# Kernel tuning notes

Hardware: AMD Instinct MI355X
Metric: run time of the kernel (lower is better)

## Reference

```python
import jax, jax.numpy as jnp
import numpy as np

EPS_NORM = 1e-12
EPS_COS = 1e-8

def _l2norm(x, axis):
    n = jnp.linalg.norm(x, axis=axis, keepdims=True)
    return x / jnp.maximum(n, EPS_NORM)

def setup_inputs() -> dict:
    key = jax.random.key(0)
    k1, k2, k3 = jax.random.split(key, 3)
    B, C, H, W, M = 16, 512, 32, 32, 1024
    query = jax.random.normal(k1, (B, C, H, W), dtype=jnp.float32)
    keys = jax.random.normal(k2, (M, C), dtype=jnp.float32)
    entropy = jax.random.uniform(k3, (B * H * W, 1), dtype=jnp.float32) + 1e-3
    return {"query": query, "keys": keys, "entropy": entropy}

def reference(query, keys, entropy):
    B, C, H, W = query.shape
    M = keys.shape[0]
    N = B * H * W
    # F.normalize over channel dim, then BCHW -> BHWC -> [N, C]
    q = _l2norm(query, axis=1)
    q = jnp.transpose(q, (0, 2, 3, 1))
    qr = q.reshape(N, C)

    # get_score: softmax over queries (axis 0) and over memory (axis 1)
    score = jnp.einsum('nd,md->nm', qr, keys)  # [N, M]
    sq = jax.nn.softmax(score, axis=0)
    sm = jax.nn.softmax(score, axis=1)

    # ---- memory_loss ----
    argm = jnp.argmax(sm, axis=1)               # topk(k=1) over memory
    closest = keys[argm]                         # [N, C]
    eye = jnp.eye(M, dtype=keys.dtype)
    gram = keys @ keys.T
    diversity_loss = jnp.sum((gram * (1.0 - eye)) ** 2) / (M * M - M)
    cos = jnp.sum(qr * closest, axis=1) / jnp.maximum(
        jnp.linalg.norm(qr, axis=1) * jnp.linalg.norm(closest, axis=1), EPS_COS)
    similarity_loss = jnp.dot(1.0 - cos, entropy[:, 0])  # CosineEmbeddingLoss(target=1) . entropy

    # ---- read ----
    concat_memory = jax.lax.stop_gradient(sm) @ keys    # [N, C]
    updated_query = jnp.concatenate([qr, concat_memory], axis=1)  # [N, 2C]
    updated_query = updated_query.reshape(B, H, W, 2 * C)
    updated_query = jnp.transpose(updated_query, (0, 3, 1, 2))    # [B, 2C, H, W]

    # ---- update (train=True) ----
    g = argm                                     # gathering indices (argmax == topk1)
    sq_d = jax.lax.stop_gradient(sq)
    ent_d = jax.lax.stop_gradient(entropy[:, 0])
    colmax = jnp.max(sq_d, axis=0)               # max score per memory slot [M]
    w = (sq_d[jnp.arange(N), g] / colmax[g]) * (ent_d / jnp.max(ent_d))  # [N]
    query_update = jax.ops.segment_sum(w[:, None] * qr, g, num_segments=M)  # [M, C]
    updated_memory = _l2norm(query_update + jax.lax.stop_gradient(keys), axis=1)
    gram2 = updated_memory @ updated_memory.T
    diversity_loss_updated = jnp.sum((gram2 * (1.0 - eye)) ** 2) / (M * M - M)
    updated_memory = jax.lax.stop_gradient(updated_memory)

    return (updated_query, updated_memory, sq, sm, diversity_loss_updated, similarity_loss)
```

## Files before the change

kernel.cpp:

```cpp
#include <hip/hip_runtime.h>

typedef unsigned int  u32;
typedef unsigned short u16;
typedef __bf16 bf16x8 __attribute__((ext_vector_type(8)));
typedef float  f32x4  __attribute__((ext_vector_type(4)));

#define O1 16777216
#define O2 17301504
#define O3 34078720
#define O4 50855936
#define O5 50855937

#define WS_QHI   0u
#define WS_QLO   16777216u
#define WS_KHI   33554432u
#define WS_KLO   34603008u
#define WS_KT    35651584u
#define WS_KNORM 36700160u
#define WS_CNT   36704256u
#define WS_OFFS  36708352u
#define WS_CUR   36712704u
#define WS_RN    36769792u
#define WS_PMAX  36835328u
#define WS_PSUM  36900864u
#define WS_CMAX  36966400u
#define WS_CSUM  36970496u
#define WS_ARGM  36974592u
#define WS_WGT   37040128u
#define WS_SCAL  39202816u

__device__ __forceinline__ u16 bf_rne(float f){
  u32 u = __float_as_uint(f);
  u32 r = u + 0x7fffu + ((u >> 16) & 1u);
  return (u16)(r >> 16);
}
__device__ __forceinline__ float bf_f(u16 h){ return __uint_as_float(((u32)h) << 16); }

__device__ __forceinline__ void glds16(const void* g, void* l){
  __builtin_amdgcn_global_load_lds((const __attribute__((address_space(1))) u32*)g,
                                   (__attribute__((address_space(3))) u32*)l, 16, 0, 0);
}

__global__ void k_init(u32* count, float* scal){
  int i = blockIdx.x*256 + threadIdx.x;
  if (i < 1024) count[i] = 0u;
  if (i < 16) scal[i] = 0.f;
}

__global__ __launch_bounds__(64) void k_keys(const float* __restrict__ keys,
    u16* __restrict__ khi, u16* __restrict__ klo, float* __restrict__ knorm){
  int m = blockIdx.x, l = threadIdx.x;
  const float* kr = keys + (size_t)m*512 + l*8;
  float f[8];
  #pragma unroll
  for (int i=0;i<8;i++) f[i] = kr[i];
  float ss = 0.f;
  #pragma unroll
  for (int i=0;i<8;i++) ss += f[i]*f[i];
  for (int o=32;o>0;o>>=1) ss += __shfl_xor(ss,o);
  if (l == 0) knorm[m] = sqrtf(ss);
  u32 hh[4], ll[4];
  #pragma unroll
  for (int i=0;i<4;i++){
    u16 h0 = bf_rne(f[2*i]);   u16 l0 = bf_rne(f[2*i]   - bf_f(h0));
    u16 h1 = bf_rne(f[2*i+1]); u16 l1 = bf_rne(f[2*i+1] - bf_f(h1));
    hh[i] = (u32)h0 | ((u32)h1<<16);
    ll[i] = (u32)l0 | ((u32)l1<<16);
  }
  *(uint4*)&khi[(size_t)m*512 + l*8] = make_uint4(hh[0],hh[1],hh[2],hh[3]);
  *(uint4*)&klo[(size_t)m*512 + l*8] = make_uint4(ll[0],ll[1],ll[2],ll[3]);
}

__global__ __launch_bounds__(256) void k_keysT(const float* __restrict__ keys, u16* __restrict__ kT){
  __shared__ float t2[64*65];
  int m0 = blockIdx.x*64, c0 = blockIdx.y*64;
  int t = threadIdx.x; int j = t & 63; int ig = t >> 6;
  #pragma unroll 4
  for (int ii=0; ii<16; ++ii){
    int i = ig*16 + ii;
    t2[i*65 + j] = keys[(size_t)(m0+i)*512 + c0 + j];
  }
  __syncthreads();
  #pragma unroll 4
  for (int ii=0; ii<16; ++ii){
    int i = ig*16 + ii;
    kT[(size_t)(c0+i)*1024 + m0 + j] = bf_rne(t2[j*65 + i]);
  }
}

__global__ __launch_bounds__(256) void k_maxent(const float* __restrict__ ent, float* scal){
  int i = blockIdx.x*512 + threadIdx.x;
  float v = fmaxf(ent[i], ent[i + 256]);
  for (int o=32;o>0;o>>=1) v = fmaxf(v, __shfl_xor(v,o));
  __shared__ float r4[4];
  if ((threadIdx.x & 63) == 0) r4[threadIdx.x>>6] = v;
  __syncthreads();
  if (threadIdx.x == 0){
    float mx = fmaxf(fmaxf(r4[0],r4[1]), fmaxf(r4[2],r4[3]));
    atomicMax((u32*)(scal + 1), __float_as_uint(mx));
  }
}

__global__ __launch_bounds__(256) void k_phaseA(const float* __restrict__ query, float* __restrict__ out0,
    u16* __restrict__ qhi, u16* __restrict__ qlo, float* __restrict__ rn_g){
  __shared__ float tile[64*65];
  __shared__ float red[256];
  __shared__ float sinv[64];
  int bx = blockIdx.x; int b = bx >> 4; int hw0 = (bx & 15)*64;
  int t = threadIdx.x; int hw = t & 63; int cg = t >> 6;
  const float* qb = query + (size_t)b*524288 + hw0 + hw;
  float p = 0.f;
  for (int c = cg; c < 512; c += 4){ float v = qb[(size_t)c*1024]; p += v*v; }
  red[cg*64 + hw] = p;
  __syncthreads();
  if (t < 64){
    float ss = red[t] + red[64+t] + red[128+t] + red[192+t];
    float nrm = sqrtf(ss);
    float inv = 1.0f / fmaxf(nrm, 1e-12f);
    sinv[t] = inv;
    rn_g[b*1024 + hw0 + t] = nrm * inv;
  }
  __syncthreads();
  int nl = t >> 2, cq = t & 3;
  int n = b*1024 + hw0 + nl;
  float invv = sinv[hw];
  for (int cb = 0; cb < 8; ++cb){
    int cbase = cb*64;
    #pragma unroll 4
    for (int i = 0; i < 16; ++i){
      int cl = cg*16 + i;
      int c = cbase + cl;
      float v = query[(size_t)b*524288 + (size_t)c*1024 + hw0 + hw] * invv;
      tile[cl*65 + hw] = v;
      out0[(size_t)b*1048576 + (size_t)c*1024 + hw0 + hw] = v;
    }
    __syncthreads();
    u32 hh[8], ll[8];
    #pragma unroll
    for (int p2 = 0; p2 < 8; ++p2){
      float f0 = tile[(cq*16 + p2*2)*65 + nl];
      float f1 = tile[(cq*16 + p2*2 + 1)*65 + nl];
      u16 h0 = bf_rne(f0); u16 lo0 = bf_rne(f0 - bf_f(h0));
      u16 h1 = bf_rne(f1); u16 lo1 = bf_rne(f1 - bf_f(h1));
      hh[p2] = (u32)h0 | ((u32)h1 << 16);
      ll[p2] = (u32)lo0 | ((u32)lo1 << 16);
    }
    size_t base = (size_t)n*512 + cbase + cq*16;
    *(uint4*)&qhi[base]     = make_uint4(hh[0],hh[1],hh[2],hh[3]);
    *(uint4*)&qhi[base + 8] = make_uint4(hh[4],hh[5],hh[6],hh[7]);
    *(uint4*)&qlo[base]     = make_uint4(ll[0],ll[1],ll[2],ll[3]);
    *(uint4*)&qlo[base + 8] = make_uint4(ll[4],ll[5],ll[6],ll[7]);
    __syncthreads();
  }
}

__global__ __launch_bounds__(256) void k_score(const u16* __restrict__ qhi, const u16* __restrict__ qlo,
    const u16* __restrict__ khi, const u16* __restrict__ klo, float* __restrict__ S){
  __shared__ u16 sAh[8192], sAl[8192], sBh[8192], sBl[8192];
  int tid = threadIdx.x;
  int nt = blockIdx.x >> 3, mt = blockIdx.x & 7;
  int nBase = nt*128, mBase = mt*128;
  int wave = tid >> 6, lane = tid & 63;
  int rw = (wave>>1)*64, cw = (wave&1)*64;
  int m16 = lane & 15, q4 = lane >> 4;
  f32x4 acc[4][4] = {};
  int srow = tid >> 3, sg = tid & 7;
  for (int kit = 0; kit < 8; ++kit){
    int k0 = kit*64;
    #pragma unroll
    for (int it = 0; it < 4; ++it){
      int row = it*32 + srow;
      int gsw = (sg ^ (row & 7)) * 8;
      int lo = it*2048 + tid*8;
      glds16(qhi + (size_t)(nBase + row)*512 + k0 + gsw, &sAh[lo]);
      glds16(qlo + (size_t)(nBase + row)*512 + k0 + gsw, &sAl[lo]);
      glds16(khi + (size_t)(mBase + row)*512 + k0 + gsw, &sBh[lo]);
      glds16(klo + (size_t)(mBase + row)*512 + k0 + gsw, &sBl[lo]);
    }
    __syncthreads();
    #pragma unroll
    for (int ks = 0; ks < 2; ++ks){
      bf16x8 a0[4], a1[4], b0[4], b1[4];
      int g = ks*4 + q4;
      #pragma unroll
      for (int i=0;i<4;i++){
        int r = rw + i*16 + m16;
        int off = r*64 + (g ^ (r&7))*8;
        a0[i] = *(const bf16x8*)&sAh[off];
        a1[i] = *(const bf16x8*)&sAl[off];
      }
      #pragma unroll
      for (int j=0;j<4;j++){
        int r = cw + j*16 + m16;
        int off = r*64 + (g ^ (r&7))*8;
        b0[j] = *(const bf16x8*)&sBh[off];
        b1[j] = *(const bf16x8*)&sBl[off];
      }
      #pragma unroll
      for (int i=0;i<4;i++)
        #pragma unroll
        for (int j=0;j<4;j++){
          acc[i][j] = __builtin_amdgcn_mfma_f32_16x16x32_bf16(a0[i], b0[j], acc[i][j], 0,0,0);
          acc[i][j] = __builtin_amdgcn_mfma_f32_16x16x32_bf16(a0[i], b1[j], acc[i][j], 0,0,0);
          acc[i][j] = __builtin_amdgcn_mfma_f32_16x16x32_bf16(a1[i], b0[j], acc[i][j], 0,0,0);
        }
    }
    __syncthreads();
  }
  #pragma unroll
  for (int i=0;i<4;i++){
    int rbase = nBase + rw + i*16 + q4*4;
    #pragma unroll
    for (int j=0;j<4;j++){
      int col = mBase + cw + j*16 + m16;
      #pragma unroll
      for (int r=0;r<4;r++)
        S[(size_t)(rbase + r)*1024 + col] = acc[i][j][r];
    }
  }
}

__global__ __launch_bounds__(256) void k_colstat(const float* __restrict__ S,
    float* __restrict__ pmax, float* __restrict__ psum){
  int c = threadIdx.x & 63;
  int col = blockIdx.x*64 + c;
  int rg = threadIdx.x >> 6;
  int row0 = blockIdx.y*1024 + rg*256;
  float m = -3.4e38f, s = 0.f;
  for (int r=0;r<256;r++){
    float v = S[(size_t)(row0+r)*1024 + col];
    if (v > m){ s = s*__expf(m - v) + 1.f; m = v; }
    else s += __expf(v - m);
  }
  __shared__ float lm[256], ls[256];
  lm[rg*64 + c] = m; ls[rg*64 + c] = s;
  __syncthreads();
  if (threadIdx.x < 64){
    int t = threadIdx.x;
    float M = lm[t];
    for (int g2=1; g2<4; ++g2) M = fmaxf(M, lm[g2*64+t]);
    float st = 0.f;
    for (int g2=0; g2<4; ++g2) st += ls[g2*64+t]*__expf(lm[g2*64+t] - M);
    pmax[blockIdx.y*1024 + blockIdx.x*64 + t] = M;
    psum[blockIdx.y*1024 + blockIdx.x*64 + t] = st;
  }
}

__global__ void k_colfin(const float* __restrict__ pmax, const float* __restrict__ psum,
    float* __restrict__ cmax, float* __restrict__ csum){
  int col = blockIdx.x*256 + threadIdx.x;
  float M = -3.4e38f, s = 0.f;
  for (int ch=0; ch<16; ++ch){
    float mi = pmax[ch*1024 + col], si = psum[ch*1024 + col];
    float nm = fmaxf(M, mi);
    s = s*__expf(M - nm) + si*__expf(mi - nm);
    M = nm;
  }
  cmax[col] = M; csum[col] = s;
}

__global__ __launch_bounds__(256) void k_row(float* __restrict__ S, float* __restrict__ sm,
    const float* __restrict__ cmax, const float* __restrict__ csum,
    const float* __restrict__ rn, const float* __restrict__ knorm,
    const float* __restrict__ ent, const float* __restrict__ scal,
    int* __restrict__ argm, float* __restrict__ wgt, u32* __restrict__ count,
    float* __restrict__ sim_acc){
  int wave = threadIdx.x >> 6, lane = threadIdx.x & 63;
  int n = blockIdx.x*4 + wave;
  float4 v[4];
  const float4* Sr = (const float4*)(S + (size_t)n*1024);
  #pragma unroll
  for (int j=0;j<4;j++) v[j] = Sr[j*64 + lane];
  float m = -3.4e38f; int gi = 0;
  #pragma unroll
  for (int j=0;j<4;j++){
    int c0 = j*256 + lane*4;
    if (v[j].x > m){ m=v[j].x; gi=c0; }
    if (v[j].y > m){ m=v[j].y; gi=c0+1; }
    if (v[j].z > m){ m=v[j].z; gi=c0+2; }
    if (v[j].w > m){ m=v[j].w; gi=c0+3; }
  }
  for (int o=32;o>0;o>>=1){
    float om = __shfl_xor(m,o); int oi = __shfl_xor(gi,o);
    if (om > m || (om == m && oi < gi)){ m = om; gi = oi; }
  }
  float4 e[4]; float s = 0.f;
  #pragma unroll
  for (int j=0;j<4;j++){
    e[j].x = __expf(v[j].x - m); e[j].y = __expf(v[j].y - m);
    e[j].z = __expf(v[j].z - m); e[j].w = __expf(v[j].w - m);
    s += e[j].x + e[j].y + e[j].z + e[j].w;
  }
  for (int o=32;o>0;o>>=1) s += __shfl_xor(s,o);
  float ri = 1.f/s;
  float4* smr = (float4*)(sm + (size_t)n*1024);
  #pragma unroll
  for (int j=0;j<4;j++){
    float4 t2; t2.x=e[j].x*ri; t2.y=e[j].y*ri; t2.z=e[j].z*ri; t2.w=e[j].w*ri;
    smr[j*64 + lane] = t2;
  }
  float4* sqr = (float4*)(S + (size_t)n*1024);
  #pragma unroll
  for (int j=0;j<4;j++){
    int c0 = j*256 + lane*4;
    float4 cm = *(const float4*)(cmax + c0);
    float4 cs = *(const float4*)(csum + c0);
    float4 q;
    q.x = __expf(v[j].x - cm.x)/cs.x;
    q.y = __expf(v[j].y - cm.y)/cs.y;
    q.z = __expf(v[j].z - cm.z)/cs.z;
    q.w = __expf(v[j].w - cm.w)/cs.w;
    sqr[j*64 + lane] = q;
  }
  __shared__ float simw[4];
  if (lane == 0){
    float en = ent[n];
    float cosv = m / fmaxf(rn[n]*knorm[gi], 1e-8f);
    simw[wave] = (1.f - cosv)*en;
    float w = __expf(m - cmax[gi]) * en / scal[1];
    wgt[n] = w; argm[n] = gi;
    atomicAdd(&count[gi], 1u);
  }
  __syncthreads();
  if (threadIdx.x == 0)
    atomicAdd(sim_acc, simw[0]+simw[1]+simw[2]+simw[3]);
}

__global__ __launch_bounds__(256) void k_scan(const u32* __restrict__ count,
    u32* __restrict__ offs, u32* __restrict__ cursor){
  int t = threadIdx.x;
  u32 v0 = count[t*4], v1 = count[t*4+1], v2 = count[t*4+2], v3 = count[t*4+3];
  u32 s = v0+v1+v2+v3;
  u32 x = s;
  for (int o=1;o<64;o<<=1){ u32 y = __shfl_up(x,o); if ((t&63) >= o) x += y; }
  __shared__ u32 wsum[4];
  if ((t&63) == 63) wsum[t>>6] = x;
  __syncthreads();
  u32 wb = 0;
  for (int wv=0; wv < (t>>6); ++wv) wb += wsum[wv];
  u32 excl = wb + x - s;
  u32 o0 = excl, o1 = excl+v0, o2 = excl+v0+v1, o3 = excl+v0+v1+v2;
  offs[t*4]=o0; offs[t*4+1]=o1; offs[t*4+2]=o2; offs[t*4+3]=o3;
  cursor[t*4]=o0; cursor[t*4+1]=o1; cursor[t*4+2]=o2; cursor[t*4+3]=o3;
  if (t == 255) offs[1024] = 16384u;
}

__global__ __launch_bounds__(256) void k_bucket(const int* __restrict__ argm,
    u32* __restrict__ cursor, u32* __restrict__ list){
  int n = blockIdx.x*256 + threadIdx.x;
  int g = argm[n];
  u32 pos = atomicAdd(&cursor[g], 1u);
  list[pos] = n;
}

__global__ __launch_bounds__(128) void k_gather(const u16* __restrict__ qhi, const u16* __restrict__ qlo,
    const u32* __restrict__ offs, const u32* __restrict__ list, const float* __restrict__ wgt,
    const float* __restrict__ keys, float* __restrict__ out1, float* __restrict__ scal){
  int m = blockIdx.x, t = threadIdx.x;
  int c0 = t*4;
  float a0=0.f,a1=0.f,a2=0.f,a3=0.f;
  u32 beg = offs[m], end = offs[m+1];
  for (u32 r = beg; r < end; ++r){
    int n = (int)list[r];
    float w = wgt[n];
    uint2 hh = *(const uint2*)&qhi[(size_t)n*512 + c0];
    uint2 ll = *(const uint2*)&qlo[(size_t)n*512 + c0];
    float f0 = bf_f((u16)(hh.x & 0xffffu)) + bf_f((u16)(ll.x & 0xffffu));
    float f1 = bf_f((u16)(hh.x >> 16))     + bf_f((u16)(ll.x >> 16));
    float f2 = bf_f((u16)(hh.y & 0xffffu)) + bf_f((u16)(ll.y & 0xffffu));
    float f3 = bf_f((u16)(hh.y >> 16))     + bf_f((u16)(ll.y >> 16));
    a0 += w*f0; a1 += w*f1; a2 += w*f2; a3 += w*f3;
  }
  float4 k4 = *(const float4*)(keys + (size_t)m*512 + c0);
  float u0 = a0 + k4.x, u1 = a1 + k4.y, u2 = a2 + k4.z, u3 = a3 + k4.w;
  float ss = u0*u0 + u1*u1 + u2*u2 + u3*u3;
  for (int o=32;o>0;o>>=1) ss += __shfl_xor(ss,o);
  __shared__ float r2[2];
  if ((t&63) == 0) r2[t>>6] = ss;
  __syncthreads();
  float tot = r2[0] + r2[1];
  float inv = 1.f / fmaxf(sqrtf(tot), 1e-12f);
  float4 o4; o4.x=u0*inv; o4.y=u1*inv; o4.z=u2*inv; o4.w=u3*inv;
  *(float4*)(out1 + (size_t)m*512 + c0) = o4;
  if (t == 0){
    float s2 = tot*inv*inv;
    atomicAdd(scal + 3, s2*s2);
  }
}

__global__ __launch_bounds__(256) void k_concat(const u16* __restrict__ kT, const float* __restrict__ sm,
    float* __restrict__ out0){
  __shared__ u16 sA[8192];
  __shared__ u16 sB[128*72];
  int tid = threadIdx.x;
  int ct = blockIdx.x & 3, nt = blockIdx.x >> 2;
  int cBase = ct*128, nBase = nt*128;
  int wave = tid>>6, lane = tid&63;
  int rw = (wave>>1)*64, cw = (wave&1)*64;
  int m16 = lane&15, q4 = lane>>4;
  f32x4 acc[4][4] = {};
  int srow = tid>>3, sg = tid&7;
  int nl = tid>>1, half = tid&1;
  for (int kit=0; kit<16; ++kit){
    int k0 = kit*64;
    #pragma unroll
    for (int it=0; it<4; ++it){
      int row = it*32 + srow;
      int gsw = (sg ^ (row & 7)) * 8;
      glds16(kT + (size_t)(cBase + row)*1024 + k0 + gsw, &sA[it*2048 + tid*8]);
    }
    {
      const float* src = sm + (size_t)(nBase + nl)*1024 + k0 + half*32;
      float4 f[8];
      #pragma unroll
      for (int q=0;q<8;q++) f[q] = *(const float4*)(src + q*4);
      u16* dst = &sB[nl*72 + half*32];
      #pragma unroll
      for (int q=0;q<4;q++){
        const float* fp = (const float*)&f[q*2];
        u32 w0 = (u32)bf_rne(fp[0]) | ((u32)bf_rne(fp[1])<<16);
        u32 w1 = (u32)bf_rne(fp[2]) | ((u32)bf_rne(fp[3])<<16);
        u32 w2 = (u32)bf_rne(fp[4]) | ((u32)bf_rne(fp[5])<<16);
        u32 w3 = (u32)bf_rne(fp[6]) | ((u32)bf_rne(fp[7])<<16);
        *(uint4*)(dst + q*8) = make_uint4(w0,w1,w2,w3);
      }
    }
    __syncthreads();
    #pragma unroll
    for (int ks=0; ks<2; ++ks){
      bf16x8 a[4], b[4];
      int g = ks*4 + q4;
      #pragma unroll
      for (int i=0;i<4;i++){
        int r = rw + i*16 + m16;
        a[i] = *(const bf16x8*)&sA[r*64 + (g ^ (r&7))*8];
      }
      #pragma unroll
      for (int j=0;j<4;j++){
        int r = cw + j*16 + m16;
        b[j] = *(const bf16x8*)&sB[r*72 + ks*32 + q4*8];
      }
      #pragma unroll
      for (int i=0;i<4;i++)
        #pragma unroll
        for (int j=0;j<4;j++)
          acc[i][j] = __builtin_amdgcn_mfma_f32_16x16x32_bf16(a[i], b[j], acc[i][j], 0,0,0);
    }
    __syncthreads();
  }
  #pragma unroll
  for (int i=0;i<4;i++){
    int c = cBase + rw + i*16 + q4*4;
    #pragma unroll
    for (int j=0;j<4;j++){
      int n = nBase + cw + j*16 + m16;
      int b2 = n >> 10, hw = n & 1023;
      #pragma unroll
      for (int r=0;r<4;r++)
        out0[(size_t)b2*1048576 + (size_t)(512 + c + r)*1024 + hw] = acc[i][j][r];
    }
  }
}

__global__ __launch_bounds__(256) void k_gram(const float* __restrict__ U, float* __restrict__ scal){
  __shared__ float Ua[64*34], Ub[64*34];
  int bx = blockIdx.x & 15, by = blockIdx.x >> 4;
  int t = threadIdx.x;
  int c1 = (t >> 4)*2, c2 = (t & 15)*2;
  float d00=0,d01=0,d10=0,d11=0;
  for (int ch=0; ch<16; ++ch){
    #pragma unroll
    for (int j=0;j<8;j++){
      int flat = j*256 + t;
      int ml = flat >> 5, c = flat & 31;
      Ua[ml*34 + c] = U[(size_t)(ch*64 + ml)*512 + bx*32 + c];
      Ub[ml*34 + c] = U[(size_t)(ch*64 + ml)*512 + by*32 + c];
    }
    __syncthreads();
    #pragma unroll 8
    for (int ml=0; ml<64; ++ml){
      float2 a = *(const float2*)&Ua[ml*34 + c1];
      float2 b = *(const float2*)&Ub[ml*34 + c2];
      d00 += a.x*b.x; d01 += a.x*b.y; d10 += a.y*b.x; d11 += a.y*b.y;
    }
    __syncthreads();
  }
  float loc = d00*d00 + d01*d01 + d10*d10 + d11*d11;
  for (int o=32;o>0;o>>=1) loc += __shfl_xor(loc,o);
  __shared__ float r4[4];
  if ((t&63) == 0) r4[t>>6] = loc;
  __syncthreads();
  if (t == 0) atomicAdd(scal + 2, r4[0]+r4[1]+r4[2]+r4[3]);
}

__global__ void k_final(const float* __restrict__ scal, float* __restrict__ out){
  out[O4] = (scal[2] - scal[3]) * (1.0f/1047552.0f);
  out[O5] = scal[0];
}

extern "C" void kernel_launch(void* const* d_in, const int* in_sizes, int n_in,
                              void* d_out, int out_size, void* d_ws, size_t ws_size,
                              hipStream_t stream) {
  const float* query = (const float*)d_in[0];
  const float* keys  = (const float*)d_in[1];
  const float* ent   = (const float*)d_in[2];
  float* out  = (float*)d_out;
  char*  ws   = (char*)d_ws;

  u16*   qhi   = (u16*)(ws + WS_QHI);
  u16*   qlo   = (u16*)(ws + WS_QLO);
  u16*   khi   = (u16*)(ws + WS_KHI);
  u16*   klo   = (u16*)(ws + WS_KLO);
  u16*   kT    = (u16*)(ws + WS_KT);
  float* knorm = (float*)(ws + WS_KNORM);
  u32*   count = (u32*)(ws + WS_CNT);
  u32*   offs  = (u32*)(ws + WS_OFFS);
  u32*   cursor= (u32*)(ws + WS_CUR);
  float* rn    = (float*)(ws + WS_RN);
  float* pmax  = (float*)(ws + WS_PMAX);
  float* psum  = (float*)(ws + WS_PSUM);
  float* cmax  = (float*)(ws + WS_CMAX);
  float* csum  = (float*)(ws + WS_CSUM);
  int*   argm  = (int*)(ws + WS_ARGM);
  float* wgt   = (float*)(ws + WS_WGT);
  float* scal  = (float*)(ws + WS_SCAL);
  u32*   list  = (u32*)(ws + WS_PMAX);

  float* S   = out + O2;
  float* sm  = out + O3;
  float* um  = out + O1;

  k_init   <<<4,    256, 0, stream>>>(count, scal);
  k_keys   <<<1024,  64, 0, stream>>>(keys, khi, klo, knorm);
  k_keysT  <<<dim3(16,8), 256, 0, stream>>>(keys, kT);
  k_maxent <<<32,   256, 0, stream>>>(ent, scal);
  k_phaseA <<<256,  256, 0, stream>>>(query, out, qhi, qlo, rn);
  k_score  <<<1024, 256, 0, stream>>>(qhi, qlo, khi, klo, S);
  k_colstat<<<dim3(16,16), 256, 0, stream>>>(S, pmax, psum);
  k_colfin <<<4,    256, 0, stream>>>(pmax, psum, cmax, csum);
  k_row    <<<4096, 256, 0, stream>>>(S, sm, cmax, csum, rn, knorm, ent, scal, argm, wgt, count, scal );
  k_scan   <<<1,    256, 0, stream>>>(count, offs, cursor);
  k_bucket <<<64,   256, 0, stream>>>(argm, cursor, list);
  k_gather <<<1024, 128, 0, stream>>>(qhi, qlo, offs, list, wgt, keys, um, scal);
  k_concat <<<512,  256, 0, stream>>>(kT, sm, out);
  k_gram   <<<256,  256, 0, stream>>>(um, scal);
  k_final  <<<1,      1, 0, stream>>>(scal, out);
}
```

Baseline: 588.9 us.

## Fuse column softmax stats into score GEMM epilogue; feed concat with bf16 sm copy

Per-tile column max and sum-of-exp are now computed in the k_score epilogue from the accumulators and written as 128 partial chunks. This removes the separate k_colstat pass that re-read the full 64MB score matrix. k_row also writes a bf16 copy of sm, so k_concat can load it directly into LDS with async global_load_lds instead of reading fp32 and converting inside the GEMM loop. The cost is an extra 32MB bf16 write, a longer k_colfin reduction over 128 chunks, and a heavier epilogue in k_score.

```diff
diff --git a/kernel.cpp b/kernel.cpp
--- a/kernel.cpp
+++ b/kernel.cpp
@@ -22,12 +22,14 @@
 #define WS_CUR   36712704u
 #define WS_RN    36769792u
 #define WS_PMAX  36835328u
-#define WS_PSUM  36900864u
 #define WS_CMAX  36966400u
 #define WS_CSUM  36970496u
 #define WS_ARGM  36974592u
 #define WS_WGT   37040128u
 #define WS_SCAL  39202816u
+#define WS_PM2   39203840u
+#define WS_PS2   39728128u
+#define WS_SM16  40252416u
 
 __device__ __forceinline__ u16 bf_rne(float f){
   u32 u = __float_as_uint(f);
@@ -155,7 +157,8 @@
 }
 
 __global__ __launch_bounds__(256) void k_score(const u16* __restrict__ qhi, const u16* __restrict__ qlo,
-    const u16* __restrict__ khi, const u16* __restrict__ klo, float* __restrict__ S){
+    const u16* __restrict__ khi, const u16* __restrict__ klo, float* __restrict__ S,
+    float* __restrict__ pm2, float* __restrict__ ps2){
   __shared__ u16 sAh[8192], sAl[8192], sBh[8192], sBl[8192];
   int tid = threadIdx.x;
   int nt = blockIdx.x >> 3, mt = blockIdx.x & 7;
@@ -218,40 +221,50 @@
         S[(size_t)(rbase + r)*1024 + col] = acc[i][j][r];
     }
   }
-}
-
-__global__ __launch_bounds__(256) void k_colstat(const float* __restrict__ S,
-    float* __restrict__ pmax, float* __restrict__ psum){
-  int c = threadIdx.x & 63;
-  int col = blockIdx.x*64 + c;
-  int rg = threadIdx.x >> 6;
-  int row0 = blockIdx.y*1024 + rg*256;
-  float m = -3.4e38f, s = 0.f;
-  for (int r=0;r<256;r++){
-    float v = S[(size_t)(row0+r)*1024 + col];
-    if (v > m){ s = s*__expf(m - v) + 1.f; m = v; }
-    else s += __expf(v - m);
-  }
-  __shared__ float lm[256], ls[256];
-  lm[rg*64 + c] = m; ls[rg*64 + c] = s;
-  __syncthreads();
-  if (threadIdx.x < 64){
-    int t = threadIdx.x;
-    float M = lm[t];
-    for (int g2=1; g2<4; ++g2) M = fmaxf(M, lm[g2*64+t]);
-    float st = 0.f;
-    for (int g2=0; g2<4; ++g2) st += ls[g2*64+t]*__expf(lm[g2*64+t] - M);
-    pmax[blockIdx.y*1024 + blockIdx.x*64 + t] = M;
-    psum[blockIdx.y*1024 + blockIdx.x*64 + t] = st;
-  }
-}
-
-__global__ void k_colfin(const float* __restrict__ pmax, const float* __restrict__ psum,
+  float* lm = (float*)sAh;
+  float* ls = lm + 256;
+  #pragma unroll
+  for (int j=0;j<4;j++){
+    float cm = -3.4e38f;
+    #pragma unroll
+    for (int i=0;i<4;i++)
+      #pragma unroll
+      for (int r=0;r<4;r++) cm = fmaxf(cm, acc[i][j][r]);
+    cm = fmaxf(cm, __shfl_xor(cm, 16));
+    cm = fmaxf(cm, __shfl_xor(cm, 32));
+    float cs = 0.f;
+    #pragma unroll
+    for (int i=0;i<4;i++)
+      #pragma unroll
+      for (int r=0;r<4;r++) cs += __expf(acc[i][j][r] - cm);
+    cs += __shfl_xor(cs, 16);
+    cs += __shfl_xor(cs, 32);
+    if (lane < 16){
+      lm[(wave*4 + j)*16 + m16] = cm;
+      ls[(wave*4 + j)*16 + m16] = cs;
+    }
+  }
+  __syncthreads();
+  if (tid < 128){
+    int w = tid >> 6;
+    int x = tid & 63;
+    int j = x >> 4, c16 = x & 15;
+    float m0 = lm[(w*4 + j)*16 + c16],     s0 = ls[(w*4 + j)*16 + c16];
+    float m1 = lm[((w+2)*4 + j)*16 + c16], s1 = ls[((w+2)*4 + j)*16 + c16];
+    float M  = fmaxf(m0, m1);
+    float Sv = s0*__expf(m0 - M) + s1*__expf(m1 - M);
+    int col = mBase + w*64 + j*16 + c16;
+    pm2[nt*1024 + col] = M;
+    ps2[nt*1024 + col] = Sv;
+  }
+}
+
+__global__ void k_colfin(const float* __restrict__ pm2, const float* __restrict__ ps2,
     float* __restrict__ cmax, float* __restrict__ csum){
   int col = blockIdx.x*256 + threadIdx.x;
   float M = -3.4e38f, s = 0.f;
-  for (int ch=0; ch<16; ++ch){
-    float mi = pmax[ch*1024 + col], si = psum[ch*1024 + col];
+  for (int ch=0; ch<128; ++ch){
+    float mi = pm2[ch*1024 + col], si = ps2[ch*1024 + col];
     float nm = fmaxf(M, mi);
     s = s*__expf(M - nm) + si*__expf(mi - nm);
     M = nm;
@@ -260,6 +273,7 @@
 }
 
 __global__ __launch_bounds__(256) void k_row(float* __restrict__ S, float* __restrict__ sm,
+    u16* __restrict__ sm16,
     const float* __restrict__ cmax, const float* __restrict__ csum,
     const float* __restrict__ rn, const float* __restrict__ knorm,
     const float* __restrict__ ent, const float* __restrict__ scal,
@@ -298,6 +312,9 @@
   for (int j=0;j<4;j++){
     float4 t2; t2.x=e[j].x*ri; t2.y=e[j].y*ri; t2.z=e[j].z*ri; t2.w=e[j].w*ri;
     smr[j*64 + lane] = t2;
+    u32 w0 = (u32)bf_rne(t2.x) | ((u32)bf_rne(t2.y) << 16);
+    u32 w1 = (u32)bf_rne(t2.z) | ((u32)bf_rne(t2.w) << 16);
+    *(uint2*)&sm16[(size_t)n*1024 + j*256 + lane*4] = make_uint2(w0, w1);
   }
   float4* sqr = (float4*)(S + (size_t)n*1024);
   #pragma unroll
@@ -388,10 +405,10 @@
   }
 }
 
-__global__ __launch_bounds__(256) void k_concat(const u16* __restrict__ kT, const float* __restrict__ sm,
+__global__ __launch_bounds__(256) void k_concat(const u16* __restrict__ kT, const u16* __restrict__ sm16,
     float* __restrict__ out0){
   __shared__ u16 sA[8192];
-  __shared__ u16 sB[128*72];
+  __shared__ u16 sB[8192];
   int tid = threadIdx.x;
   int ct = blockIdx.x & 3, nt = blockIdx.x >> 2;
   int cBase = ct*128, nBase = nt*128;
@@ -400,30 +417,15 @@
   int m16 = lane&15, q4 = lane>>4;
   f32x4 acc[4][4] = {};
   int srow = tid>>3, sg = tid&7;
-  int nl = tid>>1, half = tid&1;
   for (int kit=0; kit<16; ++kit){
     int k0 = kit*64;
     #pragma unroll
     for (int it=0; it<4; ++it){
       int row = it*32 + srow;
       int gsw = (sg ^ (row & 7)) * 8;
-      glds16(kT + (size_t)(cBase + row)*1024 + k0 + gsw, &sA[it*2048 + tid*8]);
-    }
-    {
-      const float* src = sm + (size_t)(nBase + nl)*1024 + k0 + half*32;
-      float4 f[8];
-      #pragma unroll
-      for (int q=0;q<8;q++) f[q] = *(const float4*)(src + q*4);
-      u16* dst = &sB[nl*72 + half*32];
-      #pragma unroll
-      for (int q=0;q<4;q++){
-        const float* fp = (const float*)&f[q*2];
-        u32 w0 = (u32)bf_rne(fp[0]) | ((u32)bf_rne(fp[1])<<16);
-        u32 w1 = (u32)bf_rne(fp[2]) | ((u32)bf_rne(fp[3])<<16);
-        u32 w2 = (u32)bf_rne(fp[4]) | ((u32)bf_rne(fp[5])<<16);
-        u32 w3 = (u32)bf_rne(fp[6]) | ((u32)bf_rne(fp[7])<<16);
-        *(uint4*)(dst + q*8) = make_uint4(w0,w1,w2,w3);
-      }
+      int lo = it*2048 + tid*8;
+      glds16(kT   + (size_t)(cBase + row)*1024 + k0 + gsw, &sA[lo]);
+      glds16(sm16 + (size_t)(nBase + row)*1024 + k0 + gsw, &sB[lo]);
     }
     __syncthreads();
     #pragma unroll
@@ -438,7 +440,7 @@
       #pragma unroll
       for (int j=0;j<4;j++){
         int r = cw + j*16 + m16;
-        b[j] = *(const bf16x8*)&sB[r*72 + ks*32 + q4*8];
+        b[j] = *(const bf16x8*)&sB[r*64 + (g ^ (r&7))*8];
       }
       #pragma unroll
       for (int i=0;i<4;i++)
@@ -517,14 +519,15 @@
   u32*   offs  = (u32*)(ws + WS_OFFS);
   u32*   cursor= (u32*)(ws + WS_CUR);
   float* rn    = (float*)(ws + WS_RN);
-  float* pmax  = (float*)(ws + WS_PMAX);
-  float* psum  = (float*)(ws + WS_PSUM);
   float* cmax  = (float*)(ws + WS_CMAX);
   float* csum  = (float*)(ws + WS_CSUM);
   int*   argm  = (int*)(ws + WS_ARGM);
   float* wgt   = (float*)(ws + WS_WGT);
   float* scal  = (float*)(ws + WS_SCAL);
   u32*   list  = (u32*)(ws + WS_PMAX);
+  float* pm2   = (float*)(ws + WS_PM2);
+  float* ps2   = (float*)(ws + WS_PS2);
+  u16*   sm16  = (u16*)(ws + WS_SM16);
 
   float* S   = out + O2;
   float* sm  = out + O3;
@@ -535,14 +538,13 @@
   k_keysT  <<<dim3(16,8), 256, 0, stream>>>(keys, kT);
   k_maxent <<<32,   256, 0, stream>>>(ent, scal);
   k_phaseA <<<256,  256, 0, stream>>>(query, out, qhi, qlo, rn);
-  k_score  <<<1024, 256, 0, stream>>>(qhi, qlo, khi, klo, S);
-  k_colstat<<<dim3(16,16), 256, 0, stream>>>(S, pmax, psum);
-  k_colfin <<<4,    256, 0, stream>>>(pmax, psum, cmax, csum);
-  k_row    <<<4096, 256, 0, stream>>>(S, sm, cmax, csum, rn, knorm, ent, scal, argm, wgt, count, scal );
+  k_score  <<<1024, 256, 0, stream>>>(qhi, qlo, khi, klo, S, pm2, ps2);
+  k_colfin <<<4,    256, 0, stream>>>(pm2, ps2, cmax, csum);
+  k_row    <<<4096, 256, 0, stream>>>(S, sm, sm16, cmax, csum, rn, knorm, ent, scal, argm, wgt, count, scal );
   k_scan   <<<1,    256, 0, stream>>>(count, offs, cursor);
   k_bucket <<<64,   256, 0, stream>>>(argm, cursor, list);
   k_gather <<<1024, 128, 0, stream>>>(qhi, qlo, offs, list, wgt, keys, um, scal);
-  k_concat <<<512,  256, 0, stream>>>(kT, sm, out);
+  k_concat <<<512,  256, 0, stream>>>(kT, sm16, out);
   k_gram   <<<256,  256, 0, stream>>>(um, scal);
   k_final  <<<1,      1, 0, stream>>>(scal, out);
 }
```

Result: faster. 515.4 us (-12.5%).
